# Kernel optimization log

Hardware: AMD Instinct MI355X
Metric: run time of the kernel (lower is better)

Reference implementation:

```python
import jax, jax.numpy as jnp
import numpy as np

B, T, IN_DIM, OUT_DIM = 1024, 64, 8, 2
H, K, HIDDEN = 3, 5, 256
LOG_STD_MIN, LOG_STD_MAX = -20.0, 2.0


def setup_inputs() -> dict:
    key = jax.random.key(0)
    ks = jax.random.split(key, 12)
    def lin(k, fan_in, fan_out):
        b = 1.0 / np.sqrt(fan_in)
        return jax.random.uniform(k, (fan_in, fan_out), jnp.float32, -b, b)
    inp = {
        'state': jax.random.normal(ks[0], (B, T, IN_DIM), jnp.float32),
        'noise': jax.random.normal(ks[1], (B, T, OUT_DIM), jnp.float32),
        'Wq': lin(ks[2], IN_DIM, K * H),
        'Wk': lin(ks[3], K, K * H),
        'Wv': lin(ks[4], K, K * H),
        'W1': lin(ks[5], K * H + IN_DIM, HIDDEN),
        'b1': jnp.zeros((HIDDEN,), jnp.float32),
        'W2': lin(ks[6], HIDDEN, HIDDEN),
        'b2': jnp.zeros((HIDDEN,), jnp.float32),
        'Wmu': jax.random.uniform(ks[7], (HIDDEN, OUT_DIM), jnp.float32, -0.003, 0.003),
        'bmu': jax.random.uniform(ks[8], (OUT_DIM,), jnp.float32, -0.003, 0.003),
        'Wls': jax.random.uniform(ks[9], (HIDDEN, OUT_DIM), jnp.float32, -0.003, 0.003),
        'bls': jax.random.uniform(ks[10], (OUT_DIM,), jnp.float32, -0.003, 0.003),
    }
    return inp


# static off-diagonal neighbor indices: row i -> all j != i
_OFFDIAG = np.array([[j for j in range(T) if j != i] for i in range(T)], dtype=np.int32)


def _forward(state, noise, Wq, Wk, Wv, W1, b1, W2, b2, Wmu, bmu, Wls, bls):
    b, t, _ = state.shape
    # rel[b,i,j] = state[b,j,:4] - state[b,i,:4]
    rel4 = state[:, None, :, 0:4] - state[:, :, None, 0:4]          # [b,t,t,4] (x,y,vx,vy)
    x_comp = rel4[..., 0::2]                                         # [x, vx]
    y_comp = rel4[..., 1::2]                                         # [y, vy]
    ang = (-state[:, :, 7] + 0.5 * jnp.pi)[:, None, :, None]         # varies with j (own-ref of key agent)
    c, s = jnp.cos(ang), jnp.sin(ang)
    xn = x_comp * c - y_comp * s                                     # [x', vx']
    yn = x_comp * s + y_comp * c                                     # [y', vy']
    rel = jnp.stack([xn[..., 0], yn[..., 0], xn[..., 1], yn[..., 1]], axis=-1)  # [b,t,t,4]
    # drop self-pairs (diagonal) -> [b,t,t-1,4]
    idx = jnp.asarray(_OFFDIAG)
    rel_od = rel[:, jnp.arange(t)[:, None], idx]
    r = jnp.sqrt(rel_od[..., 0] ** 2 + rel_od[..., 1] ** 2)[..., None]   # [b,t,t-1,1]
    r_trans = jax.nn.sigmoid(1.0 - 5.0 * (r - 0.2))                       # 1/(1+exp(-1+5(r-0.2)))
    rel_n = jnp.concatenate([rel_od[..., 0:2] / r, rel_od[..., 2:4], r_trans], axis=-1)  # [b,t,t-1,5]
    h, k = H, K
    q = (state @ Wq).reshape(b, t, h, k)                              # [b,t,h,k]
    keys = (rel_n @ Wk).reshape(b, t, t - 1, h, k)                    # [b,t,n,h,k]
    vals = (rel_n @ Wv).reshape(b, t, t - 1, h, k)
    scores = jnp.einsum('btnhk,bthk->bthn', keys, q) / jnp.sqrt(jnp.float32(k))
    w = jax.nn.softmax(scores, axis=-1)                               # over t-1 neighbors
    att = jnp.einsum('bthn,btnhk->bthk', w, vals).reshape(b, t, h * k)
    x = jnp.concatenate([att, state], axis=-1)
    x = jax.nn.relu(x @ W1 + b1)
    x = jax.nn.relu(x @ W2 + b2)
    mu = jnp.tanh(x @ Wmu + bmu)
    log_std = jnp.tanh(x @ Wls + bls)
    log_std = LOG_STD_MIN + 0.5 * (LOG_STD_MAX - LOG_STD_MIN) * (log_std + 1.0)
    std = jnp.exp(log_std)
    z = mu + std * noise                                              # rsample with explicit noise
    action = jnp.tanh(z)
    # Normal(mu,std).log_prob(z) with (z-mu)/std == noise
    log_prob = -0.5 * noise ** 2 - log_std - 0.5 * jnp.log(2.0 * jnp.pi)
    log_prob = log_prob - jnp.log(1.0 - action ** 2 + 1e-7)
    log_prob = jnp.sum(log_prob, axis=-1, keepdims=True)
    return action, log_prob


def reference(state, noise, Wq, Wk, Wv, W1, b1, W2, b2, Wmu, bmu, Wls, bls):
    return _forward(state, noise, Wq, Wk, Wv, W1, b1, W2, b2, Wmu, bmu, Wls, bls)
```

## Files before the change

kernel.cpp:

```cpp
#include <hip/hip_runtime.h>
#include <math.h>

#define NROWS 65536

typedef short bf16x8 __attribute__((ext_vector_type(8)));
typedef float f32x4  __attribute__((ext_vector_type(4)));
typedef float f32x2  __attribute__((ext_vector_type(2)));

__device__ __forceinline__ unsigned short f2bf(float x){
    unsigned int u = __float_as_uint(x);
    u += 0x7FFFu + ((u >> 16) & 1u);
    return (unsigned short)(u >> 16);
}
__device__ __forceinline__ f32x2 sp2(float x){ return (f32x2){x, x}; }

template<int CTRL, int RM>
__device__ __forceinline__ float dpp_add(float v){
    int m = __builtin_amdgcn_update_dpp(0, __float_as_int(v), CTRL, RM, 0xF, 1);
    return v + __int_as_float(m);
}
__device__ __forceinline__ float rowsum16(float v){
    v = dpp_add<0x111, 0xF>(v);
    v = dpp_add<0x112, 0xF>(v);
    v = dpp_add<0x114, 0xF>(v);
    v = dpp_add<0x118, 0xF>(v);
    return v;
}
__device__ __forceinline__ float bfly8_add(float v){
    v = dpp_add<0xB1, 0xF>(v);
    v = dpp_add<0x4E, 0xF>(v);
    v = dpp_add<0x141, 0xF>(v);
    return v;
}

__global__ __launch_bounds__(256) void prep_kernel(
    const float* __restrict__ W2, const float* __restrict__ W1,
    unsigned short* __restrict__ w2frag, unsigned short* __restrict__ w1frag)
{
    const int bx = blockIdx.x, t = threadIdx.x;
    if (bx < 128){
        const int ct = bx >> 3, kk = bx & 7;
        #pragma unroll
        for (int s = 0; s < 2; ++s){
            int f = t * 2 + s;
            int lane = f >> 3, e = f & 7;
            int k = kk * 32 + (lane >> 4) * 8 + e;
            int c = ct * 16 + (lane & 15);
            w2frag[(size_t)(ct * 8 + kk) * 512 + f] = f2bf(W2[k * 256 + c]);
        }
    } else {
        #pragma unroll
        for (int s = 0; s < 32; ++s){
            int flat = t * 32 + s;
            int ct = flat >> 9, r = flat & 511;
            int lane = r >> 3, e = r & 7;
            int k = (lane >> 4) * 8 + e;
            int c = ct * 16 + (lane & 15);
            w1frag[flat] = (k < 23) ? f2bf(W1[k * 256 + c]) : (unsigned short)0;
        }
    }
}

__global__ __launch_bounds__(512, 4) void actor_kernel(
    const float* __restrict__ state, const float* __restrict__ noise,
    const float* __restrict__ Wq, const float* __restrict__ Wk,
    const float* __restrict__ Wv,
    const unsigned short* __restrict__ w1frag, const float* __restrict__ b1,
    const unsigned short* __restrict__ w2frag, const float* __restrict__ b2,
    const float* __restrict__ Wmu, const float* __restrict__ bmu,
    const float* __restrict__ Wls, const float* __restrict__ bls,
    float* __restrict__ action_out, float* __restrict__ logprob_out)
{
    __shared__ __align__(16) unsigned char uniA[64 * 264 * 2];
    float* sLDS  = (float*)uniA;
    float* pjLDS = sLDS + 576;
    float* qkLDS = pjLDS + 384;
    unsigned short* h1LDS = (unsigned short*)uniA;
    __shared__ __align__(16) unsigned short x0LDS[64 * 40];
    __shared__ float headLDS[8 * 64 * 5];

    const int t    = threadIdx.x;
    const int lane = t & 63;
    const int w    = t >> 6;
    const int lm   = lane & 15;
    const int lq   = lane >> 4;
    const int b    = blockIdx.x;

    {
        float v = state[(size_t)b * 512 + t];
        int r = t >> 3, c = t & 7;
        sLDS[r * 9 + c] = v;
        if (c < 4) pjLDS[(r & 31) * 12 + c * 2 + (r >> 5)] = v;
    }
    __syncthreads();

    if (t < 192){
        const int row = t & 63, h = t >> 6;
        float s[8];
        #pragma unroll
        for (int d = 0; d < 8; ++d) s[d] = sLDS[row * 9 + d];
        float q[5];
        #pragma unroll
        for (int e = 0; e < 5; ++e){
            int m = h * 5 + e;
            float acc = 0.f;
            #pragma unroll
            for (int d = 0; d < 8; ++d) acc += s[d] * Wq[d * 15 + m];
            q[e] = acc;
        }
        #pragma unroll
        for (int f = 0; f < 5; ++f){
            float acc = 0.f;
            #pragma unroll
            for (int kk = 0; kk < 5; ++kk) acc += Wk[f * 15 + h * 5 + kk] * q[kk];
            qkLDS[row * 17 + h * 5 + f] = acc * 0.64519834f;
        }
    } else if (w == 7){
        const int row = lane;
        float ang = 1.5707963267948966f - sLDS[row * 9 + 7];
        float sn, cs;
        __sincosf(ang, &sn, &cs);
        int base = (row & 31) * 12 + (row >> 5);
        pjLDS[base + 8]  = sn;
        pjLDS[base + 10] = cs;
    }
    __syncthreads();

    {
        const int il = lane >> 3;
        const int js = lane & 7;
        const int i  = w * 8 + il;
        const float si0 = sLDS[i * 9 + 0], si1 = sLDS[i * 9 + 1];
        const float si2 = sLDS[i * 9 + 2], si3 = sLDS[i * 9 + 3];
        float qkv[15];
        #pragma unroll
        for (int m = 0; m < 15; ++m) qkv[m] = qkLDS[i * 17 + m];

        f32x2 s0 = {0.f,0.f}, s1 = {0.f,0.f}, s2 = {0.f,0.f};
        f32x2 g0[5], g1[5], g2[5];
        #pragma unroll
        for (int f = 0; f < 5; ++f){ g0[f] = sp2(0.f); g1[f] = sp2(0.f); g2[f] = sp2(0.f); }

        #pragma unroll
        for (int jj = 0; jj < 4; ++jj){
            const int jb = jj * 8 + js;
            const f32x2* pp = (const f32x2*)&pjLDS[jb * 12];
            f32x2 p0 = pp[0], p1 = pp[1], p2 = pp[2], p3 = pp[3];
            f32x2 sn = pp[4], cs = pp[5];
            f32x2 d0 = p0 - sp2(si0), d1 = p1 - sp2(si1);
            f32x2 d2 = p2 - sp2(si2), d3 = p3 - sp2(si3);
            f32x2 xn0 = d0 * cs - d1 * sn, yn0 = d0 * sn + d1 * cs;
            f32x2 xn1 = d2 * cs - d3 * sn, yn1 = d2 * sn + d3 * cs;
            f32x2 r2v = xn0 * xn0 + yn0 * yn0;
            const bool self0 = (jb == i), self1 = (jb + 32 == i);
            f32x2 inv_r;
            inv_r.x = self0 ? 0.f : rsqrtf(r2v.x);
            inv_r.y = self1 ? 0.f : rsqrtf(r2v.y);
            f32x2 rv  = r2v * inv_r;
            f32x2 arg = rv * sp2(7.2134752f) - sp2(2.8853901f);
            f32x2 ex; ex.x = exp2f(arg.x); ex.y = exp2f(arg.y);
            f32x2 f4; f4.x = 1.f / (1.f + ex.x); f4.y = 1.f / (1.f + ex.y);
            f32x2 f0 = xn0 * inv_r, f1 = yn0 * inv_r;
            f32x2 sc0 = f0*sp2(qkv[0])  + f1*sp2(qkv[1])  + xn1*sp2(qkv[2])  + yn1*sp2(qkv[3])  + f4*sp2(qkv[4]);
            f32x2 sc1 = f0*sp2(qkv[5])  + f1*sp2(qkv[6])  + xn1*sp2(qkv[7])  + yn1*sp2(qkv[8])  + f4*sp2(qkv[9]);
            f32x2 sc2 = f0*sp2(qkv[10]) + f1*sp2(qkv[11]) + xn1*sp2(qkv[12]) + yn1*sp2(qkv[13]) + f4*sp2(qkv[14]);
            f32x2 e0, e1, e2;
            e0.x = self0 ? 0.f : exp2f(sc0.x);  e0.y = self1 ? 0.f : exp2f(sc0.y);
            e1.x = self0 ? 0.f : exp2f(sc1.x);  e1.y = self1 ? 0.f : exp2f(sc1.y);
            e2.x = self0 ? 0.f : exp2f(sc2.x);  e2.y = self1 ? 0.f : exp2f(sc2.y);
            s0 += e0; s1 += e1; s2 += e2;
            g0[0] += e0*f0; g0[1] += e0*f1; g0[2] += e0*xn1; g0[3] += e0*yn1; g0[4] += e0*f4;
            g1[0] += e1*f0; g1[1] += e1*f1; g1[2] += e1*xn1; g1[3] += e1*yn1; g1[4] += e1*f4;
            g2[0] += e2*f0; g2[1] += e2*f1; g2[2] += e2*xn1; g2[3] += e2*yn1; g2[4] += e2*f4;
        }
        float S0 = s0.x + s0.y, S1 = s1.x + s1.y, S2 = s2.x + s2.y;
        float G0[5], G1[5], G2[5];
        #pragma unroll
        for (int f = 0; f < 5; ++f){
            G0[f] = bfly8_add(g0[f].x + g0[f].y);
            G1[f] = bfly8_add(g1[f].x + g1[f].y);
            G2[f] = bfly8_add(g2[f].x + g2[f].y);
        }
        S0 = bfly8_add(S0); S1 = bfly8_add(S1); S2 = bfly8_add(S2);
        float i0 = 1.f / S0, i1 = 1.f / S1, i2 = 1.f / S2;

        #pragma unroll
        for (int mm = 0; mm < 2; ++mm){
            int m = js * 2 + mm;
            if (m < 15){
                float A0 = (m < 5) ? G0[0] : (m < 10) ? G1[0] : G2[0];
                float A1 = (m < 5) ? G0[1] : (m < 10) ? G1[1] : G2[1];
                float A2 = (m < 5) ? G0[2] : (m < 10) ? G1[2] : G2[2];
                float A3 = (m < 5) ? G0[3] : (m < 10) ? G1[3] : G2[3];
                float A4 = (m < 5) ? G0[4] : (m < 10) ? G1[4] : G2[4];
                float I  = (m < 5) ? i0    : (m < 10) ? i1    : i2;
                float av = (A0 * Wv[m] + A1 * Wv[15 + m] + A2 * Wv[30 + m]
                          + A3 * Wv[45 + m] + A4 * Wv[60 + m]) * I;
                x0LDS[i * 40 + m] = f2bf(av);
            }
        }
        x0LDS[i * 40 + 15 + js] = f2bf(sLDS[i * 9 + js]);
        x0LDS[i * 40 + 23 + js] = 0;
        if (js == 0) x0LDS[i * 40 + 31] = 0;
    }
    __syncthreads();

    {
        bf16x8 afr[4];
        #pragma unroll
        for (int rt = 0; rt < 4; ++rt)
            afr[rt] = *(const bf16x8*)&x0LDS[(rt * 16 + lm) * 40 + lq * 8];
        #pragma unroll
        for (int ci = 0; ci < 2; ++ci){
            const int ct = w * 2 + ci;
            bf16x8 bfr = *(const bf16x8*)&w1frag[(size_t)ct * 512 + lane * 8];
            float bb = b1[ct * 16 + lm];
            #pragma unroll
            for (int rt = 0; rt < 4; ++rt){
                f32x4 c0 = {0.f, 0.f, 0.f, 0.f};
                c0 = __builtin_amdgcn_mfma_f32_16x16x32_bf16(afr[rt], bfr, c0, 0, 0, 0);
                #pragma unroll
                for (int p = 0; p < 4; ++p)
                    h1LDS[(rt * 16 + lq * 4 + p) * 264 + ct * 16 + lm] = f2bf(fmaxf(c0[p] + bb, 0.f));
            }
        }
    }
    __syncthreads();

    {
        f32x4 acc[4][2];
        #pragma unroll
        for (int rt = 0; rt < 4; ++rt)
            #pragma unroll
            for (int ci = 0; ci < 2; ++ci) acc[rt][ci] = (f32x4){0.f, 0.f, 0.f, 0.f};

        #pragma unroll
        for (int kk = 0; kk < 8; ++kk){
            bf16x8 arf[4], brf[2];
            #pragma unroll
            for (int rt = 0; rt < 4; ++rt)
                arf[rt] = *(const bf16x8*)&h1LDS[(rt * 16 + lm) * 264 + kk * 32 + lq * 8];
            #pragma unroll
            for (int ci = 0; ci < 2; ++ci)
                brf[ci] = *(const bf16x8*)&w2frag[(size_t)((w * 2 + ci) * 8 + kk) * 512 + lane * 8];
            #pragma unroll
            for (int rt = 0; rt < 4; ++rt)
                #pragma unroll
                for (int ci = 0; ci < 2; ++ci)
                    acc[rt][ci] = __builtin_amdgcn_mfma_f32_16x16x32_bf16(arf[rt], brf[ci], acc[rt][ci], 0, 0, 0);
        }

        float bb[2];
        float2 wm[2], wl[2];
        #pragma unroll
        for (int ci = 0; ci < 2; ++ci){
            int c = (w * 2 + ci) * 16 + lm;
            bb[ci] = b2[c];
            wm[ci] = *(const float2*)&Wmu[c * 2];
            wl[ci] = *(const float2*)&Wls[c * 2];
        }
        #pragma unroll
        for (int rt = 0; rt < 4; ++rt){
            #pragma unroll
            for (int p = 0; p < 4; ++p){
                float m0 = 0.f, m1 = 0.f, l0 = 0.f, l1 = 0.f;
                #pragma unroll
                for (int ci = 0; ci < 2; ++ci){
                    float hv = fmaxf(acc[rt][ci][p] + bb[ci], 0.f);
                    m0 += hv * wm[ci].x;
                    m1 += hv * wm[ci].y;
                    l0 += hv * wl[ci].x;
                    l1 += hv * wl[ci].y;
                }
                m0 = rowsum16(m0); m1 = rowsum16(m1);
                l0 = rowsum16(l0); l1 = rowsum16(l1);
                if (lm == 15){
                    int row = rt * 16 + lq * 4 + p;
                    float* hp = &headLDS[(w * 64 + row) * 5];
                    hp[0] = m0; hp[1] = m1; hp[2] = l0; hp[3] = l1;
                }
            }
        }
    }
    __syncthreads();

    if (t < 64){
        const int row = t;
        float m0 = 0.f, m1 = 0.f, l0 = 0.f, l1 = 0.f;
        #pragma unroll
        for (int ww = 0; ww < 8; ++ww){
            const float* hp = &headLDS[(ww * 64 + row) * 5];
            m0 += hp[0]; m1 += hp[1]; l0 += hp[2]; l1 += hp[3];
        }
        const size_t grow = (size_t)b * 64 + row;
        float n0 = noise[grow * 2 + 0];
        float n1 = noise[grow * 2 + 1];
        float lp = 0.f;
        {
            float mu = tanhf(m0 + bmu[0]);
            float ls = tanhf(l0 + bls[0]);
            ls = -20.f + 11.f * (ls + 1.f);
            float sd = expf(ls);
            float a = tanhf(mu + sd * n0);
            action_out[grow * 2 + 0] = a;
            lp += -0.5f * n0 * n0 - ls - 0.9189385332046727f - logf(1.f - a * a + 1e-7f);
        }
        {
            float mu = tanhf(m1 + bmu[1]);
            float ls = tanhf(l1 + bls[1]);
            ls = -20.f + 11.f * (ls + 1.f);
            float sd = expf(ls);
            float a = tanhf(mu + sd * n1);
            action_out[grow * 2 + 1] = a;
            lp += -0.5f * n1 * n1 - ls - 0.9189385332046727f - logf(1.f - a * a + 1e-7f);
        }
        logprob_out[grow] = lp;
    }
}

extern "C" void kernel_launch(void* const* d_in, const int* in_sizes, int n_in,
                              void* d_out, int out_size, void* d_ws, size_t ws_size,
                              hipStream_t stream)
{
    (void)in_sizes; (void)n_in; (void)out_size; (void)ws_size;
    const float* state = (const float*)d_in[0];
    const float* noise = (const float*)d_in[1];
    const float* Wq  = (const float*)d_in[2];
    const float* Wk  = (const float*)d_in[3];
    const float* Wv  = (const float*)d_in[4];
    const float* W1  = (const float*)d_in[5];
    const float* b1  = (const float*)d_in[6];
    const float* W2  = (const float*)d_in[7];
    const float* b2  = (const float*)d_in[8];
    const float* Wmu = (const float*)d_in[9];
    const float* bmu = (const float*)d_in[10];
    const float* Wls = (const float*)d_in[11];
    const float* bls = (const float*)d_in[12];

    unsigned short* w2frag = (unsigned short*)d_ws;
    unsigned short* w1frag = w2frag + 65536;

    float* action_out  = (float*)d_out;
    float* logprob_out = (float*)d_out + (size_t)NROWS * 2;

    prep_kernel<<<129, 256, 0, stream>>>(W2, W1, w2frag, w1frag);
    actor_kernel<<<1024, 512, 0, stream>>>(state, noise, Wq, Wk, Wv,
        w1frag, b1, w2frag, b2, Wmu, bmu, Wls, bls, action_out, logprob_out);
}
```

Measured before the change: 120.0 us.

## Use hardware transcendentals, transpose MFMA outputs for packed stores and vector head reduction

Replaces library rsqrt/exp2/div/tanh/log with raw AMDGPU intrinsics (rsq, exp2, rcp, log) and a fast tanh built from exp2 and rcp. Swaps MFMA operand order so each lane holds four consecutive columns, which allows packed bf16 conversion via v_cvt_pk_bf16_f32 and 8-byte LDS stores for h1. The same swap lets the head projection reduce across lq with a swizzle and shuffle instead of a 16-lane DPP rowsum. Vectorized f32x4 loads are used for qk, bias, head weights and headLDS. The fast intrinsics trade some accuracy, which matters most near tanh saturation and in the log term.

```diff
diff --git a/kernel.cpp b/kernel.cpp
--- a/kernel.cpp
+++ b/kernel.cpp
@@ -6,31 +6,39 @@
 typedef short bf16x8 __attribute__((ext_vector_type(8)));
 typedef float f32x4  __attribute__((ext_vector_type(4)));
 typedef float f32x2  __attribute__((ext_vector_type(2)));
+typedef unsigned int u32x2 __attribute__((ext_vector_type(2)));
 
 __device__ __forceinline__ unsigned short f2bf(float x){
     unsigned int u = __float_as_uint(x);
     u += 0x7FFFu + ((u >> 16) & 1u);
     return (unsigned short)(u >> 16);
 }
+__device__ __forceinline__ unsigned int pkbf(float lo, float hi){
+    unsigned int r;
+    asm("v_cvt_pk_bf16_f32 %0, %1, %2" : "=v"(r) : "v"(lo), "v"(hi));
+    return r;
+}
 __device__ __forceinline__ f32x2 sp2(float x){ return (f32x2){x, x}; }
 
 template<int CTRL, int RM>
 __device__ __forceinline__ float dpp_add(float v){
     int m = __builtin_amdgcn_update_dpp(0, __float_as_int(v), CTRL, RM, 0xF, 1);
     return v + __int_as_float(m);
-}
-__device__ __forceinline__ float rowsum16(float v){
-    v = dpp_add<0x111, 0xF>(v);
-    v = dpp_add<0x112, 0xF>(v);
-    v = dpp_add<0x114, 0xF>(v);
-    v = dpp_add<0x118, 0xF>(v);
-    return v;
 }
 __device__ __forceinline__ float bfly8_add(float v){
     v = dpp_add<0xB1, 0xF>(v);
     v = dpp_add<0x4E, 0xF>(v);
     v = dpp_add<0x141, 0xF>(v);
     return v;
+}
+__device__ __forceinline__ float red4_lq(float v){
+    v += __int_as_float(__builtin_amdgcn_ds_swizzle(__float_as_int(v), 0x401F));
+    v += __shfl_xor(v, 32, 64);
+    return v;
+}
+__device__ __forceinline__ float fast_tanh(float x){
+    float e = __builtin_amdgcn_exp2f(x * 2.8853900817779268f);
+    return 1.f - 2.f * __builtin_amdgcn_rcpf(e + 1.f);
 }
 
 __global__ __launch_bounds__(256) void prep_kernel(
@@ -77,7 +85,7 @@
     float* qkLDS = pjLDS + 384;
     unsigned short* h1LDS = (unsigned short*)uniA;
     __shared__ __align__(16) unsigned short x0LDS[64 * 40];
-    __shared__ float headLDS[8 * 64 * 5];
+    __shared__ __align__(16) float headLDS[8 * 64 * 4];
 
     const int t    = threadIdx.x;
     const int lane = t & 63;
@@ -113,7 +121,7 @@
             float acc = 0.f;
             #pragma unroll
             for (int kk = 0; kk < 5; ++kk) acc += Wk[f * 15 + h * 5 + kk] * q[kk];
-            qkLDS[row * 17 + h * 5 + f] = acc * 0.64519834f;
+            qkLDS[row * 20 + h * 5 + f] = acc * 0.64519834f;
         }
     } else if (w == 7){
         const int row = lane;
@@ -132,9 +140,11 @@
         const int i  = w * 8 + il;
         const float si0 = sLDS[i * 9 + 0], si1 = sLDS[i * 9 + 1];
         const float si2 = sLDS[i * 9 + 2], si3 = sLDS[i * 9 + 3];
-        float qkv[15];
-        #pragma unroll
-        for (int m = 0; m < 15; ++m) qkv[m] = qkLDS[i * 17 + m];
+        float qkv[16];
+        *(f32x4*)&qkv[0]  = *(const f32x4*)&qkLDS[i * 20 + 0];
+        *(f32x4*)&qkv[4]  = *(const f32x4*)&qkLDS[i * 20 + 4];
+        *(f32x4*)&qkv[8]  = *(const f32x4*)&qkLDS[i * 20 + 8];
+        *(f32x4*)&qkv[12] = *(const f32x4*)&qkLDS[i * 20 + 12];
 
         f32x2 s0 = {0.f,0.f}, s1 = {0.f,0.f}, s2 = {0.f,0.f};
         f32x2 g0[5], g1[5], g2[5];
@@ -154,20 +164,21 @@
             f32x2 r2v = xn0 * xn0 + yn0 * yn0;
             const bool self0 = (jb == i), self1 = (jb + 32 == i);
             f32x2 inv_r;
-            inv_r.x = self0 ? 0.f : rsqrtf(r2v.x);
-            inv_r.y = self1 ? 0.f : rsqrtf(r2v.y);
+            inv_r.x = self0 ? 0.f : __builtin_amdgcn_rsqf(r2v.x);
+            inv_r.y = self1 ? 0.f : __builtin_amdgcn_rsqf(r2v.y);
             f32x2 rv  = r2v * inv_r;
             f32x2 arg = rv * sp2(7.2134752f) - sp2(2.8853901f);
-            f32x2 ex; ex.x = exp2f(arg.x); ex.y = exp2f(arg.y);
-            f32x2 f4; f4.x = 1.f / (1.f + ex.x); f4.y = 1.f / (1.f + ex.y);
+            f32x2 f4;
+            f4.x = __builtin_amdgcn_rcpf(1.f + __builtin_amdgcn_exp2f(arg.x));
+            f4.y = __builtin_amdgcn_rcpf(1.f + __builtin_amdgcn_exp2f(arg.y));
             f32x2 f0 = xn0 * inv_r, f1 = yn0 * inv_r;
             f32x2 sc0 = f0*sp2(qkv[0])  + f1*sp2(qkv[1])  + xn1*sp2(qkv[2])  + yn1*sp2(qkv[3])  + f4*sp2(qkv[4]);
             f32x2 sc1 = f0*sp2(qkv[5])  + f1*sp2(qkv[6])  + xn1*sp2(qkv[7])  + yn1*sp2(qkv[8])  + f4*sp2(qkv[9]);
             f32x2 sc2 = f0*sp2(qkv[10]) + f1*sp2(qkv[11]) + xn1*sp2(qkv[12]) + yn1*sp2(qkv[13]) + f4*sp2(qkv[14]);
             f32x2 e0, e1, e2;
-            e0.x = self0 ? 0.f : exp2f(sc0.x);  e0.y = self1 ? 0.f : exp2f(sc0.y);
-            e1.x = self0 ? 0.f : exp2f(sc1.x);  e1.y = self1 ? 0.f : exp2f(sc1.y);
-            e2.x = self0 ? 0.f : exp2f(sc2.x);  e2.y = self1 ? 0.f : exp2f(sc2.y);
+            e0.x = self0 ? 0.f : __builtin_amdgcn_exp2f(sc0.x);  e0.y = self1 ? 0.f : __builtin_amdgcn_exp2f(sc0.y);
+            e1.x = self0 ? 0.f : __builtin_amdgcn_exp2f(sc1.x);  e1.y = self1 ? 0.f : __builtin_amdgcn_exp2f(sc1.y);
+            e2.x = self0 ? 0.f : __builtin_amdgcn_exp2f(sc2.x);  e2.y = self1 ? 0.f : __builtin_amdgcn_exp2f(sc2.y);
             s0 += e0; s1 += e1; s2 += e2;
             g0[0] += e0*f0; g0[1] += e0*f1; g0[2] += e0*xn1; g0[3] += e0*yn1; g0[4] += e0*f4;
             g1[0] += e1*f0; g1[1] += e1*f1; g1[2] += e1*xn1; g1[3] += e1*yn1; g1[4] += e1*f4;
@@ -182,7 +193,9 @@
             G2[f] = bfly8_add(g2[f].x + g2[f].y);
         }
         S0 = bfly8_add(S0); S1 = bfly8_add(S1); S2 = bfly8_add(S2);
-        float i0 = 1.f / S0, i1 = 1.f / S1, i2 = 1.f / S2;
+        float i0 = __builtin_amdgcn_rcpf(S0);
+        float i1 = __builtin_amdgcn_rcpf(S1);
+        float i2 = __builtin_amdgcn_rcpf(S2);
 
         #pragma unroll
         for (int mm = 0; mm < 2; ++mm){
@@ -214,14 +227,17 @@
         for (int ci = 0; ci < 2; ++ci){
             const int ct = w * 2 + ci;
             bf16x8 bfr = *(const bf16x8*)&w1frag[(size_t)ct * 512 + lane * 8];
-            float bb = b1[ct * 16 + lm];
+            f32x4 bb = *(const f32x4*)&b1[ct * 16 + lq * 4];
             #pragma unroll
             for (int rt = 0; rt < 4; ++rt){
                 f32x4 c0 = {0.f, 0.f, 0.f, 0.f};
-                c0 = __builtin_amdgcn_mfma_f32_16x16x32_bf16(afr[rt], bfr, c0, 0, 0, 0);
-                #pragma unroll
-                for (int p = 0; p < 4; ++p)
-                    h1LDS[(rt * 16 + lq * 4 + p) * 264 + ct * 16 + lm] = f2bf(fmaxf(c0[p] + bb, 0.f));
+                c0 = __builtin_amdgcn_mfma_f32_16x16x32_bf16(bfr, afr[rt], c0, 0, 0, 0);
+                float h0 = fmaxf(c0[0] + bb[0], 0.f);
+                float h1v = fmaxf(c0[1] + bb[1], 0.f);
+                float h2v = fmaxf(c0[2] + bb[2], 0.f);
+                float h3v = fmaxf(c0[3] + bb[3], 0.f);
+                u32x2 pk; pk.x = pkbf(h0, h1v); pk.y = pkbf(h2v, h3v);
+                *(u32x2*)&h1LDS[(rt * 16 + lm) * 264 + ct * 16 + lq * 4] = pk;
             }
         }
     }
@@ -247,38 +263,37 @@
             for (int rt = 0; rt < 4; ++rt)
                 #pragma unroll
                 for (int ci = 0; ci < 2; ++ci)
-                    acc[rt][ci] = __builtin_amdgcn_mfma_f32_16x16x32_bf16(arf[rt], brf[ci], acc[rt][ci], 0, 0, 0);
-        }
-
-        float bb[2];
-        float2 wm[2], wl[2];
+                    acc[rt][ci] = __builtin_amdgcn_mfma_f32_16x16x32_bf16(brf[ci], arf[rt], acc[rt][ci], 0, 0, 0);
+        }
+        f32x4 b2v[2], wmA[2], wmB[2], wlA[2], wlB[2];
         #pragma unroll
         for (int ci = 0; ci < 2; ++ci){
-            int c = (w * 2 + ci) * 16 + lm;
-            bb[ci] = b2[c];
-            wm[ci] = *(const float2*)&Wmu[c * 2];
-            wl[ci] = *(const float2*)&Wls[c * 2];
+            int cb = (w * 2 + ci) * 16 + lq * 4;
+            b2v[ci] = *(const f32x4*)&b2[cb];
+            wmA[ci] = *(const f32x4*)&Wmu[cb * 2];
+            wmB[ci] = *(const f32x4*)&Wmu[cb * 2 + 4];
+            wlA[ci] = *(const f32x4*)&Wls[cb * 2];
+            wlB[ci] = *(const f32x4*)&Wls[cb * 2 + 4];
         }
         #pragma unroll
         for (int rt = 0; rt < 4; ++rt){
-            #pragma unroll
-            for (int p = 0; p < 4; ++p){
-                float m0 = 0.f, m1 = 0.f, l0 = 0.f, l1 = 0.f;
-                #pragma unroll
-                for (int ci = 0; ci < 2; ++ci){
-                    float hv = fmaxf(acc[rt][ci][p] + bb[ci], 0.f);
-                    m0 += hv * wm[ci].x;
-                    m1 += hv * wm[ci].y;
-                    l0 += hv * wl[ci].x;
-                    l1 += hv * wl[ci].y;
-                }
-                m0 = rowsum16(m0); m1 = rowsum16(m1);
-                l0 = rowsum16(l0); l1 = rowsum16(l1);
-                if (lm == 15){
-                    int row = rt * 16 + lq * 4 + p;
-                    float* hp = &headLDS[(w * 64 + row) * 5];
-                    hp[0] = m0; hp[1] = m1; hp[2] = l0; hp[3] = l1;
-                }
+            float m0 = 0.f, m1 = 0.f, l0 = 0.f, l1 = 0.f;
+            #pragma unroll
+            for (int ci = 0; ci < 2; ++ci){
+                float hv0 = fmaxf(acc[rt][ci][0] + b2v[ci][0], 0.f);
+                float hv1 = fmaxf(acc[rt][ci][1] + b2v[ci][1], 0.f);
+                float hv2 = fmaxf(acc[rt][ci][2] + b2v[ci][2], 0.f);
+                float hv3 = fmaxf(acc[rt][ci][3] + b2v[ci][3], 0.f);
+                m0 += hv0*wmA[ci][0] + hv1*wmA[ci][2] + hv2*wmB[ci][0] + hv3*wmB[ci][2];
+                m1 += hv0*wmA[ci][1] + hv1*wmA[ci][3] + hv2*wmB[ci][1] + hv3*wmB[ci][3];
+                l0 += hv0*wlA[ci][0] + hv1*wlA[ci][2] + hv2*wlB[ci][0] + hv3*wlB[ci][2];
+                l1 += hv0*wlA[ci][1] + hv1*wlA[ci][3] + hv2*wlB[ci][1] + hv3*wlB[ci][3];
+            }
+            m0 = red4_lq(m0); m1 = red4_lq(m1);
+            l0 = red4_lq(l0); l1 = red4_lq(l1);
+            if (lq == 0){
+                f32x4 o = {m0, m1, l0, l1};
+                *(f32x4*)&headLDS[(w * 64 + rt * 16 + lm) * 4] = o;
             }
         }
     }
@@ -286,33 +301,33 @@
 
     if (t < 64){
         const int row = t;
-        float m0 = 0.f, m1 = 0.f, l0 = 0.f, l1 = 0.f;
-        #pragma unroll
-        for (int ww = 0; ww < 8; ++ww){
-            const float* hp = &headLDS[(ww * 64 + row) * 5];
-            m0 += hp[0]; m1 += hp[1]; l0 += hp[2]; l1 += hp[3];
-        }
+        f32x4 s = {0.f, 0.f, 0.f, 0.f};
+        #pragma unroll
+        for (int ww = 0; ww < 8; ++ww)
+            s += *(const f32x4*)&headLDS[(ww * 64 + row) * 4];
         const size_t grow = (size_t)b * 64 + row;
         float n0 = noise[grow * 2 + 0];
         float n1 = noise[grow * 2 + 1];
         float lp = 0.f;
         {
-            float mu = tanhf(m0 + bmu[0]);
-            float ls = tanhf(l0 + bls[0]);
+            float mu = fast_tanh(s[0] + bmu[0]);
+            float ls = fast_tanh(s[2] + bls[0]);
             ls = -20.f + 11.f * (ls + 1.f);
-            float sd = expf(ls);
-            float a = tanhf(mu + sd * n0);
+            float sd = __builtin_amdgcn_exp2f(ls * 1.4426950408889634f);
+            float a = fast_tanh(mu + sd * n0);
             action_out[grow * 2 + 0] = a;
-            lp += -0.5f * n0 * n0 - ls - 0.9189385332046727f - logf(1.f - a * a + 1e-7f);
+            lp += -0.5f * n0 * n0 - ls - 0.9189385332046727f
+                - 0.6931471805599453f * __builtin_amdgcn_logf(1.f - a * a + 1e-7f);
         }
         {
-            float mu = tanhf(m1 + bmu[1]);
-            float ls = tanhf(l1 + bls[1]);
+            float mu = fast_tanh(s[1] + bmu[1]);
+            float ls = fast_tanh(s[3] + bls[1]);
             ls = -20.f + 11.f * (ls + 1.f);
-            float sd = expf(ls);
-            float a = tanhf(mu + sd * n1);
+            float sd = __builtin_amdgcn_exp2f(ls * 1.4426950408889634f);
+            float a = fast_tanh(mu + sd * n1);
             action_out[grow * 2 + 1] = a;
-            lp += -0.5f * n1 * n1 - ls - 0.9189385332046727f - logf(1.f - a * a + 1e-7f);
+            lp += -0.5f * n1 * n1 - ls - 0.9189385332046727f
+                - 0.6931471805599453f * __builtin_amdgcn_logf(1.f - a * a + 1e-7f);
         }
         logprob_out[grow] = lp;
     }
```

After: 110.9 us. -7.5%, faster.
